# Performance work log

Hardware: AMD Instinct MI355X
Metric: run time of the kernel (lower is better)

## Reference

```python
import jax, jax.numpy as jnp
import numpy as np

E = 1024
H = 16
D = E // H  # head dim 64
B = 2
S = 2048


def setup_inputs() -> dict:
    key = jax.random.key(0)
    k1, k2, k3, k4, k5 = jax.random.split(key, 5)
    scale = 1.0 / np.sqrt(E)
    return {
        "x": jax.random.normal(k1, (B, S, E), dtype=jnp.float32),
        "W_in": jax.random.normal(k2, (E, 3 * E), dtype=jnp.float32) * scale,
        "b_in": jnp.zeros((3 * E,), dtype=jnp.float32),
        "W_out": jax.random.normal(k3, (E, E), dtype=jnp.float32) * scale,
        "b_out": jnp.zeros((E,), dtype=jnp.float32),
        "causal_mask": 1,
    }


def reference(x, W_in, b_in, W_out, b_out, causal_mask):
    b, s, e = x.shape
    qkv = x @ W_in + b_in                      # [B,S,3E]
    q, k, v = jnp.split(qkv, 3, axis=-1)
    # [B,S,E] -> [B,H,S,D]
    q = q.reshape(b, s, H, D).transpose(0, 2, 1, 3)
    k = k.reshape(b, s, H, D).transpose(0, 2, 1, 3)
    v = v.reshape(b, s, H, D).transpose(0, 2, 1, 3)
    scores = jnp.einsum("bhqd,bhkd->bhqk", q, k)
    if causal_mask:
        # mask applied before scaling in the original; -inf is scale-invariant
        mask = jnp.triu(jnp.ones((s, s), dtype=bool), k=1)
        scores = jnp.where(mask, -jnp.inf, scores)
    scores = scores / np.sqrt(D)
    weight = jax.nn.softmax(scores, axis=-1)
    out = jnp.einsum("bhqk,bhkd->bhqd", weight, v)   # [B,H,S,D]
    out = out.transpose(0, 2, 1, 3).reshape(b, s, e)
    return out @ W_out + b_out
```

## Files before the change

kernel.cpp:

```cpp
#include <hip/hip_runtime.h>
#include <hip/hip_bf16.h>
#include <cmath>

typedef __bf16 bf16;
typedef __attribute__((ext_vector_type(8))) __bf16 bf16x8;
typedef __attribute__((ext_vector_type(4))) __bf16 bf16x4;
typedef __attribute__((ext_vector_type(4))) float f32x4;
typedef __attribute__((ext_vector_type(16))) float f32x16;
typedef unsigned int u32;

constexpr int S  = 2048;
constexpr int E  = 1024;
constexpr int H  = 16;
constexpr int D  = 64;
constexpr int B  = 2;
constexpr int M  = B * S;
constexpr int N3 = 3 * E;
constexpr int NROWS = B * H * S;

static __device__ __forceinline__ void gload16(const void* g, void* l) {
  __builtin_amdgcn_global_load_lds((const __attribute__((address_space(1))) void*)g,
                                   (__attribute__((address_space(3))) void*)l, 16, 0, 0);
}

static __device__ __forceinline__ u32 pack2(float a, float b) {
  union { bf16 h[2]; u32 u; } r;
  r.h[0] = (bf16)a; r.h[1] = (bf16)b;
  return r.u;
}
typedef union { u32 w[4]; bf16x8 v; } FU;

__global__ void k_cvt(const float* __restrict__ in, bf16* __restrict__ out) {
  const int i = (blockIdx.x * blockDim.x + threadIdx.x) * 4;
  const float4 v = *(const float4*)(in + i);
  bf16x4 o = { (bf16)v.x, (bf16)v.y, (bf16)v.z, (bf16)v.w };
  *(bf16x4*)(out + i) = o;
}

__global__ void k_transpose_cvt(const float* __restrict__ in, bf16* __restrict__ out,
                                int R, int C) {
  __shared__ float t[32][33];
  const int c0 = blockIdx.x * 32, r0 = blockIdx.y * 32;
  const int tx = threadIdx.x, ty = threadIdx.y;
  #pragma unroll
  for (int j = 0; j < 32; j += 8)
    t[ty + j][tx] = in[(size_t)(r0 + ty + j) * C + c0 + tx];
  __syncthreads();
  #pragma unroll
  for (int j = 0; j < 32; j += 8)
    out[(size_t)(c0 + ty + j) * R + r0 + tx] = (bf16)t[tx][ty + j];
}

template<int EPI>
__global__ __launch_bounds__(256) void k_gemm(
    const bf16* __restrict__ A, const bf16* __restrict__ Bt,
    const float* __restrict__ bias, float* __restrict__ outF,
    bf16* __restrict__ oQ, bf16* __restrict__ oK, bf16* __restrict__ oV,
    int Kdim, int Nn)
{
  __shared__ __align__(16) char smem[65536];
  const int tid = threadIdx.x;
  const int lane = tid & 63, w = tid >> 6;
  const int lane15 = lane & 15, quad = lane >> 4;
  const int wm = w >> 1, wn = w & 1;

  const int nbx = Nn >> 7;
  const int nwg = gridDim.x;
  const int bid = blockIdx.x;
  const int swz = (bid & 7) * (nwg >> 3) + (bid >> 3);
  const int bn0 = (swz % nbx) * 128;
  const int bm0 = (swz / nbx) * 128;

  const int so0 = w * 1024 + lane * 16;
  int srow[4], slk[4];
  #pragma unroll
  for (int p = 0; p < 4; ++p) {
    const int o = p * 4096 + so0;
    const int row = o >> 7, cbyte = o & 127;
    srow[p] = row;
    slk[p] = (cbyte ^ ((row & 7) << 4)) >> 1;
  }

  f32x4 acc[4][4] = {};
  const int nkt = Kdim >> 6;

  #pragma unroll
  for (int p = 0; p < 4; ++p) {
    gload16(A  + (size_t)(bm0 + srow[p]) * Kdim + slk[p], smem +         p * 4096 + w * 1024);
    gload16(Bt + (size_t)(bn0 + srow[p]) * Kdim + slk[p], smem + 32768 + p * 4096 + w * 1024);
  }

  #pragma unroll 1
  for (int kt = 0; kt < nkt; ++kt) {
    const int cur = kt & 1;
    __builtin_amdgcn_s_barrier();
    if (kt + 1 < nkt) {
      const int k0 = (kt + 1) << 6;
      const int nb = (cur ^ 1) * 16384;
      #pragma unroll
      for (int p = 0; p < 4; ++p) {
        gload16(A  + (size_t)(bm0 + srow[p]) * Kdim + k0 + slk[p],
                smem + nb +         p * 4096 + w * 1024);
        gload16(Bt + (size_t)(bn0 + srow[p]) * Kdim + k0 + slk[p],
                smem + nb + 32768 + p * 4096 + w * 1024);
      }
      asm volatile("s_waitcnt vmcnt(8)" ::: "memory");
    } else {
      asm volatile("s_waitcnt vmcnt(0)" ::: "memory");
    }
    __builtin_amdgcn_s_barrier();

    const char* cA = smem + cur * 16384;
    const char* cB = smem + 32768 + cur * 16384;
    #pragma unroll
    for (int kk = 0; kk < 2; ++kk) {
      bf16x8 af[4], bfr[4];
      #pragma unroll
      for (int f = 0; f < 4; ++f) {
        const int ra = wm * 64 + f * 16 + lane15;
        af[f] = *(const bf16x8*)(cA + ra * 128 +
                 ((kk * 64 + (quad << 4)) ^ ((ra & 7) << 4)));
        const int rb = wn * 64 + f * 16 + lane15;
        bfr[f] = *(const bf16x8*)(cB + rb * 128 +
                 ((kk * 64 + (quad << 4)) ^ ((rb & 7) << 4)));
      }
      #pragma unroll
      for (int i = 0; i < 4; ++i)
        #pragma unroll
        for (int j = 0; j < 4; ++j)
          acc[i][j] = __builtin_amdgcn_mfma_f32_16x16x32_bf16(af[i], bfr[j], acc[i][j], 0, 0, 0);
    }
  }

  if constexpr (EPI == 1) {
    #pragma unroll
    for (int i = 0; i < 4; ++i)
      #pragma unroll
      for (int j = 0; j < 4; ++j) {
        const int n = bn0 + wn * 64 + j * 16 + lane15;
        const float bv = bias[n];
        #pragma unroll
        for (int r = 0; r < 4; ++r) {
          const int m = bm0 + wm * 64 + i * 16 + quad * 4 + r;
          outF[(size_t)m * E + n] = acc[i][j][r] + bv;
        }
      }
  } else {
    const int which = bn0 >> 10;
    const int b  = bm0 >> 11;
    const int s0 = bm0 & (S - 1);
    const int cn0 = bn0 & (E - 1);
    if (which < 2) {
      __builtin_amdgcn_s_barrier();
      char* lC = smem;
      #pragma unroll
      for (int j = 0; j < 4; ++j) {
        const int n_loc = wn * 64 + j * 16 + lane15;
        const float bv = bias[bn0 + n_loc];
        #pragma unroll
        for (int i = 0; i < 4; ++i)
          #pragma unroll
          for (int r = 0; r < 4; ++r) {
            const int m_loc = wm * 64 + i * 16 + quad * 4 + r;
            *(bf16*)(lC + m_loc * 256 + ((n_loc * 2) ^ ((m_loc & 7) << 4))) =
                (bf16)(acc[i][j][r] + bv);
          }
      }
      __builtin_amdgcn_s_barrier();
      const int h0 = cn0 >> 6;
      #pragma unroll
      for (int it = 0; it < 8; ++it) {
        const int cch = w * 64 + it * 8 + (lane >> 3);
        const int m_loc = cch >> 1, hh = cch & 1, piece = lane & 7;
        const bf16x8 vv = *(const bf16x8*)(lC + m_loc * 256 +
                          ((hh * 128 + piece * 16) ^ ((m_loc & 7) << 4)));
        if (which == 0) {
          *(bf16x8*)(oQ + ((size_t)(b * H + h0 + hh) * S + s0 + m_loc) * D + piece * 8) = vv;
        } else {
          const size_t hb = (size_t)(b * H + h0 + hh) * S * D;
          const int tile = (s0 + m_loc) >> 6;
          const int row = m_loc & 63;
          *(bf16x8*)(oK + hb + (size_t)tile * 4096 + (piece >> 1) * 1024 +
                     (row >> 5) * 512 + (32 * (piece & 1) + (row & 31)) * 8) = vv;
        }
      }
    } else {
      #pragma unroll
      for (int j = 0; j < 4; ++j) {
        const int n_loc = wn * 64 + j * 16 + lane15;
        const int cn = cn0 + n_loc;
        const int hv = cn >> 6, dd = cn & 63;
        const float bv = bias[bn0 + n_loc];
        const size_t hb = (size_t)(b * H + hv) * S * D;
        #pragma unroll
        for (int i = 0; i < 4; ++i) {
          const int scol_g = s0 + wm * 64 + i * 16 + quad * 4;
          const int vtile = scol_g >> 6;
          const int cg = (scol_g & 63) >> 3;
          bf16x4 pk = { (bf16)(acc[i][j][0] + bv), (bf16)(acc[i][j][1] + bv),
                        (bf16)(acc[i][j][2] + bv), (bf16)(acc[i][j][3] + bv) };
          *(bf16x4*)(oV + hb + (size_t)vtile * 4096 + (cg >> 1) * 1024 +
                     (dd >> 5) * 512 + (32 * (cg & 1) + (dd & 31)) * 8 +
                     (quad & 1) * 4) = pk;
        }
      }
    }
  }
}

__global__ __launch_bounds__(256, 4) void k_attn(
    const bf16* __restrict__ Qb, const bf16* __restrict__ Kf, const bf16* __restrict__ Vf,
    bf16* __restrict__ pO0, bf16* __restrict__ pO1,
    float* __restrict__ pM, float* __restrict__ pL, const int* __restrict__ cmask)
{
  __shared__ float corr_lds[4][32];
  __shared__ float lrow_lds[4][32];

  const int tid = threadIdx.x, lane = tid & 63, w = tid >> 6;
  const int h = lane >> 5, q31 = lane & 31;
  const int bh = blockIdx.x;
  const int yy = blockIdx.y;
  const int pidx = yy & 1;
  const int c = 15 - (yy >> 1);
  const int causal = cmask[0];
  const float S2 = 0.18033688011112042f;

  const bf16* Qh = Qb + (size_t)bh * S * D;
  const bf16* Kh = Kf + (size_t)bh * S * D;
  const bf16* Vh = Vf + (size_t)bh * S * D;

  const int t0 = causal ? (pidx ? (c + 1) : 0) : (pidx ? 16 : 0);
  const int t1 = causal ? (pidx ? (2 * c + 2) : (c + 1)) : (pidx ? 32 : 16);
  const int q0w = c * 128 + 32 * w;
  const int qg  = q0w + q31;
  const int t1w = causal ? min(t1, ((q0w + 31) >> 6) + 1) : t1;

  bf16x8 qf[4];
  #pragma unroll
  for (int ds = 0; ds < 4; ++ds)
    qf[ds] = *(const bf16x8*)(Qh + (size_t)qg * D + 16 * ds + 8 * h);

  f32x16 o0 = {}, o1 = {};
  float mrun = -INFINITY, lr = 0.f;

  #pragma unroll 1
  for (int t = t0; t < t1w; ++t) {
    const bf16* ktb = Kh + (size_t)t * 4096;
    const bf16* vtb = Vh + (size_t)t * 4096;

    bf16x8 kf0[4], kf1[4];
    #pragma unroll
    for (int ds = 0; ds < 4; ++ds) {
      kf0[ds] = *(const bf16x8*)(ktb + ds * 1024 +       lane * 8);
      kf1[ds] = *(const bf16x8*)(ktb + ds * 1024 + 512 + lane * 8);
    }

    f32x16 s0v = {}, s1v = {};
    __builtin_amdgcn_s_setprio(1);
    #pragma unroll
    for (int ds = 0; ds < 4; ++ds) {
      s0v = __builtin_amdgcn_mfma_f32_32x32x16_bf16(kf0[ds], qf[ds], s0v, 0, 0, 0);
      s1v = __builtin_amdgcn_mfma_f32_32x32x16_bf16(kf1[ds], qf[ds], s1v, 0, 0, 0);
    }
    __builtin_amdgcn_s_setprio(0);

    if (causal && (64 * t + 63 > q0w)) {
      #pragma unroll
      for (int rr = 0; rr < 16; ++rr) {
        const int kg = 64 * t + (rr & 3) + 8 * (rr >> 2) + 4 * h;
        if (kg > qg)      s0v[rr] = -INFINITY;
        if (kg + 32 > qg) s1v[rr] = -INFINITY;
      }
    }

    float a8[8];
    #pragma unroll
    for (int i = 0; i < 8; ++i)
      a8[i] = fmaxf(fmaxf(s0v[i], s0v[i + 8]), fmaxf(s1v[i], s1v[i + 8]));
    float tmax = fmaxf(fmaxf(fmaxf(a8[0], a8[1]), fmaxf(a8[2], a8[3])),
                       fmaxf(fmaxf(a8[4], a8[5]), fmaxf(a8[6], a8[7])));
    tmax = fmaxf(tmax, __shfl_xor(tmax, 32, 64));

    const bool nogrow = __all(tmax <= mrun);
    const float mnew = nogrow ? mrun : fmaxf(mrun, tmax);
    float corrf = 1.f;
    if (!nogrow) {
      corrf = __builtin_amdgcn_exp2f((mrun - mnew) * S2);
      corr_lds[w][q31] = corrf;
    }
    const float msc = mnew * S2;

    #pragma unroll
    for (int rr = 0; rr < 16; ++rr) {
      s0v[rr] = __builtin_amdgcn_exp2f(__builtin_fmaf(s0v[rr], S2, -msc));
      s1v[rr] = __builtin_amdgcn_exp2f(__builtin_fmaf(s1v[rr], S2, -msc));
    }

    float b8[8];
    #pragma unroll
    for (int i = 0; i < 8; ++i)
      b8[i] = (s0v[i] + s0v[i + 8]) + (s1v[i] + s1v[i + 8]);
    float psum = ((b8[0] + b8[1]) + (b8[2] + b8[3])) + ((b8[4] + b8[5]) + (b8[6] + b8[7]));
    psum += __shfl_xor(psum, 32, 64);
    lr = lr * corrf + psum;
    mrun = mnew;

    u32 pk[8][2];
    #pragma unroll
    for (int jj = 0; jj < 4; ++jj) {
      pk[jj][0]     = pack2(s0v[4 * jj],     s0v[4 * jj + 1]);
      pk[jj][1]     = pack2(s0v[4 * jj + 2], s0v[4 * jj + 3]);
      pk[jj + 4][0] = pack2(s1v[4 * jj],     s1v[4 * jj + 1]);
      pk[jj + 4][1] = pack2(s1v[4 * jj + 2], s1v[4 * jj + 3]);
    }

    if (!nogrow) {
      #pragma unroll
      for (int j = 0; j < 4; ++j) {
        const f32x4 cv = *(const f32x4*)&corr_lds[w][8 * j + 4 * h];
        #pragma unroll
        for (int sr = 0; sr < 4; ++sr) {
          o0[4 * j + sr] *= cv[sr];
          o1[4 * j + sr] *= cv[sr];
        }
      }
    }

    __builtin_amdgcn_s_setprio(1);
    #pragma unroll
    for (int ks = 0; ks < 4; ++ks) {
      u32 a0 = pk[2 * ks][0], b0 = pk[2 * ks + 1][0];
      u32 a1 = pk[2 * ks][1], b1 = pk[2 * ks + 1][1];
      asm volatile("v_permlane32_swap_b32 %0, %1" : "+v"(a0), "+v"(b0));
      asm volatile("v_permlane32_swap_b32 %0, %1" : "+v"(a1), "+v"(b1));
      FU f; f.w[0] = a0; f.w[1] = a1; f.w[2] = b0; f.w[3] = b1;
      const bf16x8 vf0 = *(const bf16x8*)(vtb + ks * 1024 +       lane * 8);
      const bf16x8 vf1 = *(const bf16x8*)(vtb + ks * 1024 + 512 + lane * 8);
      o0 = __builtin_amdgcn_mfma_f32_32x32x16_bf16(f.v, vf0, o0, 0, 0, 0);
      o1 = __builtin_amdgcn_mfma_f32_32x32x16_bf16(f.v, vf1, o1, 0, 0, 0);
    }
    __builtin_amdgcn_s_setprio(0);
  }

  if (h == 0) {
    pM[(size_t)pidx * NROWS + bh * S + qg] = mrun;
    pL[(size_t)pidx * NROWS + bh * S + qg] = lr;
  }
  lrow_lds[w][q31] = lr;
  bf16* po = pidx ? pO1 : pO0;
  #pragma unroll
  for (int j = 0; j < 4; ++j) {
    const f32x4 lv = *(const f32x4*)&lrow_lds[w][8 * j + 4 * h];
    #pragma unroll
    for (int sr = 0; sr < 4; ++sr) {
      const int rr = 4 * j + sr;
      const float inv = lv[sr] > 0.f ? 1.0f / lv[sr] : 0.f;
      const int qrow = q0w + (rr & 3) + 8 * (rr >> 2) + 4 * h;
      bf16* dst = po + ((size_t)(bh * S + qrow)) * D;
      dst[q31]      = (bf16)(o0[rr] * inv);
      dst[32 + q31] = (bf16)(o1[rr] * inv);
    }
  }
}

__global__ __launch_bounds__(256) void k_combine(
    const bf16* __restrict__ pO0, const bf16* __restrict__ pO1,
    const float* __restrict__ pM, const float* __restrict__ pL,
    bf16* __restrict__ AO)
{
  const float S2 = 0.18033688011112042f;
  const int idx = blockIdx.x * 256 + threadIdx.x;
  const int row = idx >> 3, d0 = (idx & 7) * 8;
  const float mA = pM[row], mB = pM[NROWS + row];
  const float lA = pL[row], lB = pL[NROWS + row];
  const float m = fmaxf(mA, mB);
  const float wA = lA > 0.f ? lA * __builtin_amdgcn_exp2f((mA - m) * S2) : 0.f;
  const float wB = lB > 0.f ? lB * __builtin_amdgcn_exp2f((mB - m) * S2) : 0.f;
  const float inv = 1.0f / (wA + wB);
  const bf16x8 a = *(const bf16x8*)(pO0 + (size_t)row * D + d0);
  const bf16x8 b = *(const bf16x8*)(pO1 + (size_t)row * D + d0);
  bf16x8 o;
  #pragma unroll
  for (int i = 0; i < 8; ++i)
    o[i] = (bf16)((wA * (float)a[i] + wB * (float)b[i]) * inv);
  const int bb = row >> 15, hh = (row >> 11) & 15, s = row & 2047;
  *(bf16x8*)(AO + ((size_t)(bb * S + s)) * E + hh * D + d0) = o;
}

extern "C" void kernel_launch(void* const* d_in, const int* in_sizes, int n_in,
                              void* d_out, int out_size, void* d_ws, size_t ws_size,
                              hipStream_t stream) {
  (void)in_sizes; (void)n_in; (void)out_size; (void)ws_size;
  const float* x     = (const float*)d_in[0];
  const float* W_in  = (const float*)d_in[1];
  const float* b_in  = (const float*)d_in[2];
  const float* W_out = (const float*)d_in[3];
  const float* b_out = (const float*)d_in[4];
  const int*   cmask = (const int*)d_in[5];

  char* ws = (char*)d_ws;
  bf16* xb    = (bf16*)ws; ws += (size_t)M * E * 2;
  bf16* wtin  = (bf16*)ws; ws += (size_t)N3 * E * 2;
  bf16* wtout = (bf16*)ws; ws += (size_t)E * E * 2;
  bf16* qB    = (bf16*)ws; ws += (size_t)B * H * S * D * 2;
  bf16* kF    = (bf16*)ws; ws += (size_t)B * H * S * D * 2;
  bf16* vF    = (bf16*)ws; ws += (size_t)B * H * S * D * 2;
  bf16* ao    = (bf16*)ws; ws += (size_t)M * E * 2;
  bf16* pO1   = (bf16*)ws; ws += (size_t)NROWS * D * 2;
  float* pMb  = (float*)ws; ws += (size_t)2 * NROWS * 4;
  float* pLb  = (float*)ws; ws += (size_t)2 * NROWS * 4;
  bf16* pO0   = xb;

  k_cvt<<<M * E / 1024, 256, 0, stream>>>(x, xb);
  k_transpose_cvt<<<dim3(N3 / 32, E / 32), dim3(32, 8), 0, stream>>>(W_in, wtin, E, N3);
  k_transpose_cvt<<<dim3(E / 32, E / 32), dim3(32, 8), 0, stream>>>(W_out, wtout, E, E);
  k_gemm<0><<<dim3((M / 128) * (N3 / 128)), 256, 0, stream>>>(
      xb, wtin, b_in, nullptr, qB, kF, vF, E, N3);
  k_attn<<<dim3(32, 32), 256, 0, stream>>>(qB, kF, vF, pO0, pO1, pMb, pLb, cmask);
  k_combine<<<NROWS * 8 / 256, 256, 0, stream>>>(pO0, pO1, pMb, pLb, ao);
  k_gemm<1><<<dim3((M / 128) * (E / 128)), 256, 0, stream>>>(
      ao, wtout, b_out, (float*)d_out, nullptr, nullptr, nullptr, E, E);
}
```

Baseline: 114.4 us.

## Balance causal attention work with variable per-chunk KV splits and ordered scheduling

Replaces the fixed two-way KV split per 128-query chunk with a table-driven split of one to three parts, chosen by how many KV tiles the chunk touches. A constant scheduling table orders blocks so the heaviest pieces launch first. Partial outputs and stats are stored in compact per-slot buffers, and the combine kernel merges a variable number of partials. The aim is to even out per-block work under causal masking and cut tail imbalance. The cost is extra indirection, more partial traffic for late chunks, and a combine step that now carries branches.

```diff
diff --git a/kernel.cpp b/kernel.cpp
--- a/kernel.cpp
+++ b/kernel.cpp
@@ -17,6 +17,15 @@
 constexpr int M  = B * S;
 constexpr int N3 = 3 * E;
 constexpr int NROWS = B * H * S;
+
+__constant__ int P_tab_d[16] = {1,1,1,1,1,2,2,2,2,2,2,3,3,3,3,3};
+__constant__ int S_tab_d[16] = {0,1,2,3,4,5,7,9,11,13,15,17,20,23,26,29};
+__constant__ int c_ord_d[32] = {15,15,10,10, 15,14,14,14,13,9,9,4,
+                                13,13,12,12,8,8, 12,11,11,11,7,7,3,
+                                6,6, 5,5,2, 1, 0};
+__constant__ int p_ord_d[32] = {1,2,0,1, 0,0,1,2,2,0,1,0,
+                                0,1,1,2,0,1, 0,0,1,2,0,1,0,
+                                0,1, 0,1,0, 0, 0};
 
 static __device__ __forceinline__ void gload16(const void* g, void* l) {
   __builtin_amdgcn_global_load_lds((const __attribute__((address_space(1))) void*)g,
@@ -220,8 +229,10 @@
   const int h = lane >> 5, q31 = lane & 31;
   const int bh = blockIdx.x;
   const int yy = blockIdx.y;
-  const int pidx = yy & 1;
-  const int c = 15 - (yy >> 1);
+  const int c  = c_ord_d[yy];
+  const int p  = p_ord_d[yy];
+  const int Pc = P_tab_d[c];
+  const int sslot = S_tab_d[c] + p;
   const int causal = cmask[0];
   const float S2 = 0.18033688011112042f;
 
@@ -229,8 +240,9 @@
   const bf16* Kh = Kf + (size_t)bh * S * D;
   const bf16* Vh = Vf + (size_t)bh * S * D;
 
-  const int t0 = causal ? (pidx ? (c + 1) : 0) : (pidx ? 16 : 0);
-  const int t1 = causal ? (pidx ? (2 * c + 2) : (c + 1)) : (pidx ? 32 : 16);
+  const int nt = causal ? (2 * c + 2) : (S / 64);
+  const int t0 = (p * nt) / Pc;
+  const int t1 = ((p + 1) * nt) / Pc;
   const int q0w = c * 128 + 32 * w;
   const int qg  = q0w + q31;
   const int t1w = causal ? min(t1, ((q0w + 31) >> 6) + 1) : t1;
@@ -342,12 +354,13 @@
     __builtin_amdgcn_s_setprio(0);
   }
 
+  const int slotbase = ((bh & 15) * 32 + sslot) * 128;
   if (h == 0) {
-    pM[(size_t)pidx * NROWS + bh * S + qg] = mrun;
-    pL[(size_t)pidx * NROWS + bh * S + qg] = lr;
+    pM[(size_t)(bh * 32 + sslot) * 128 + 32 * w + q31] = mrun;
+    pL[(size_t)(bh * 32 + sslot) * 128 + 32 * w + q31] = lr;
   }
   lrow_lds[w][q31] = lr;
-  bf16* po = pidx ? pO1 : pO0;
+  bf16* po = (bh < 16 ? pO0 : pO1) + (size_t)slotbase * D;
   #pragma unroll
   for (int j = 0; j < 4; ++j) {
     const f32x4 lv = *(const f32x4*)&lrow_lds[w][8 * j + 4 * h];
@@ -355,8 +368,8 @@
     for (int sr = 0; sr < 4; ++sr) {
       const int rr = 4 * j + sr;
       const float inv = lv[sr] > 0.f ? 1.0f / lv[sr] : 0.f;
-      const int qrow = q0w + (rr & 3) + 8 * (rr >> 2) + 4 * h;
-      bf16* dst = po + ((size_t)(bh * S + qrow)) * D;
+      const int qloc = 32 * w + (rr & 3) + 8 * (rr >> 2) + 4 * h;
+      bf16* dst = po + (size_t)qloc * D;
       dst[q31]      = (bf16)(o0[rr] * inv);
       dst[32 + q31] = (bf16)(o1[rr] * inv);
     }
@@ -371,19 +384,47 @@
   const float S2 = 0.18033688011112042f;
   const int idx = blockIdx.x * 256 + threadIdx.x;
   const int row = idx >> 3, d0 = (idx & 7) * 8;
-  const float mA = pM[row], mB = pM[NROWS + row];
-  const float lA = pL[row], lB = pL[NROWS + row];
-  const float m = fmaxf(mA, mB);
-  const float wA = lA > 0.f ? lA * __builtin_amdgcn_exp2f((mA - m) * S2) : 0.f;
-  const float wB = lB > 0.f ? lB * __builtin_amdgcn_exp2f((mB - m) * S2) : 0.f;
-  const float inv = 1.0f / (wA + wB);
-  const bf16x8 a = *(const bf16x8*)(pO0 + (size_t)row * D + d0);
-  const bf16x8 b = *(const bf16x8*)(pO1 + (size_t)row * D + d0);
+  const int bh = row >> 11, s = row & 2047;
+  const int c = s >> 7, local = s & 127;
+  const int Pc = P_tab_d[c], Sc = S_tab_d[c];
+  const bf16* pbase = (bh < 16 ? pO0 : pO1);
+
+  float mv[3], lv[3];
+  float m = -INFINITY;
+  #pragma unroll
+  for (int p = 0; p < 3; ++p) {
+    if (p < Pc) {
+      mv[p] = pM[(size_t)(bh * 32 + Sc + p) * 128 + local];
+      lv[p] = pL[(size_t)(bh * 32 + Sc + p) * 128 + local];
+      m = fmaxf(m, mv[p]);
+    }
+  }
+  float wsum = 0.f, wv[3];
+  #pragma unroll
+  for (int p = 0; p < 3; ++p) {
+    wv[p] = 0.f;
+    if (p < Pc && lv[p] > 0.f) {
+      wv[p] = lv[p] * __builtin_amdgcn_exp2f((mv[p] - m) * S2);
+      wsum += wv[p];
+    }
+  }
+  const float inv = 1.0f / wsum;
+  float acc[8] = {};
+  #pragma unroll
+  for (int p = 0; p < 3; ++p) {
+    if (p < Pc) {
+      const bf16x8 a = *(const bf16x8*)(pbase +
+          ((size_t)((bh & 15) * 32 + Sc + p) * 128 + local) * D + d0);
+      #pragma unroll
+      for (int i = 0; i < 8; ++i)
+        acc[i] += wv[p] * (float)a[i];
+    }
+  }
   bf16x8 o;
   #pragma unroll
   for (int i = 0; i < 8; ++i)
-    o[i] = (bf16)((wA * (float)a[i] + wB * (float)b[i]) * inv);
-  const int bb = row >> 15, hh = (row >> 11) & 15, s = row & 2047;
+    o[i] = (bf16)(acc[i] * inv);
+  const int bb = row >> 15, hh = (row >> 11) & 15;
   *(bf16x8*)(AO + ((size_t)(bb * S + s)) * E + hh * D + d0) = o;
 }
 
```

Result: faster. 108.8 us (-4.9%).
